# Performance work log

Hardware: AMD Instinct MI355X
Metric: run time of the kernel (lower is better)

Reference implementation:

```python
import jax, jax.numpy as jnp
import numpy as np

NUM_BINS = 256


def setup_inputs() -> dict:
    key = jax.random.key(0)
    x = jax.random.uniform(key, (16, 3, 1024, 1024), dtype=jnp.float32)
    return {"x": x}


def reference(x) -> jnp.ndarray:
    B, C, H, W = x.shape
    # Quantize to NUM_BINS levels (values in [0,1] so truncation == torch .long())
    x_flat = jnp.clip(x, 0.0, 1.0).reshape(B, C, H * W)
    x_q = jnp.clip((x_flat * (NUM_BINS - 1)).astype(jnp.int32), 0, NUM_BINS - 1)
    # Per-(B,C) histogram via a single flat scatter-add: offset each (b,c)
    # slice into its own NUM_BINS-wide segment of one 1-D buffer.
    offsets = (jnp.arange(B * C, dtype=jnp.int32) * NUM_BINS).reshape(B, C, 1)
    flat_idx = (x_q + offsets).reshape(-1)
    hist = jnp.zeros(B * C * NUM_BINS, dtype=jnp.float32).at[flat_idx].add(1.0)
    hist = hist.reshape(B, C, NUM_BINS)
    # CDF, normalized by total count (clamped at 1 to avoid div-by-zero)
    cdf = jnp.cumsum(hist, axis=2)
    cdf = cdf / jnp.maximum(cdf[:, :, -1:], 1.0)
    # Remap each pixel through its channel's CDF
    y_flat = jnp.take_along_axis(cdf, x_q, axis=2)
    return y_flat.reshape(B, C, H, W).astype(x.dtype)
```

## Files before the change

kernel.cpp:

```cpp
#include <hip/hip_runtime.h>

#define NB 256
#define NCH 48
#define HW (1024*1024)
#define BLOCKS_PER_CH 64
#define THREADS 256

__device__ __forceinline__ int quant255(float v) {
    v = fminf(fmaxf(v, 0.0f), 1.0f);
    int q = (int)(v * 255.0f);
    q = q < 0 ? 0 : q;
    q = q > 255 ? 255 : q;
    return q;
}

__global__ __launch_bounds__(THREADS) void hist_kernel(
    const float* __restrict__ x, unsigned int* __restrict__ ghist) {
    __shared__ unsigned int lh[NB];
    const int t = threadIdx.x;
    lh[t] = 0u;
    __syncthreads();

    const int ch  = blockIdx.x / BLOCKS_PER_CH;
    const int blk = blockIdx.x % BLOCKS_PER_CH;

    const float4* xp = (const float4*)(x + (size_t)ch * HW);
    const int n4_per_block = (HW / 4) / BLOCKS_PER_CH;
    const int base = blk * n4_per_block;

    for (int i = base + t; i < base + n4_per_block; i += THREADS) {
        float4 v = xp[i];
        atomicAdd(&lh[quant255(v.x)], 1u);
        atomicAdd(&lh[quant255(v.y)], 1u);
        atomicAdd(&lh[quant255(v.z)], 1u);
        atomicAdd(&lh[quant255(v.w)], 1u);
    }
    __syncthreads();
    if (lh[t] != 0u)
        atomicAdd(&ghist[ch * NB + t], lh[t]);
}

__global__ __launch_bounds__(THREADS) void cdf_kernel(
    const unsigned int* __restrict__ ghist, float* __restrict__ cdf) {
    __shared__ float s[NB];
    const int c = blockIdx.x, t = threadIdx.x;
    s[t] = (float)ghist[c * NB + t];
    __syncthreads();
    for (int off = 1; off < NB; off <<= 1) {
        float add = (t >= off) ? s[t - off] : 0.0f;
        __syncthreads();
        s[t] += add;
        __syncthreads();
    }
    float total = s[NB - 1];
    cdf[c * NB + t] = s[t] / fmaxf(total, 1.0f);
}

__global__ __launch_bounds__(THREADS) void remap_kernel(
    const float* __restrict__ x, const float* __restrict__ cdf,
    float* __restrict__ y) {
    __shared__ float lc[NB];
    const int t = threadIdx.x;
    const int ch  = blockIdx.x / BLOCKS_PER_CH;
    const int blk = blockIdx.x % BLOCKS_PER_CH;
    lc[t] = cdf[ch * NB + t];
    __syncthreads();

    const float4* xp = (const float4*)(x + (size_t)ch * HW);
    float4*       yp = (float4*)      (y + (size_t)ch * HW);
    const int n4_per_block = (HW / 4) / BLOCKS_PER_CH;
    const int base = blk * n4_per_block;

    for (int i = base + t; i < base + n4_per_block; i += THREADS) {
        float4 v = xp[i];
        float4 o;
        o.x = lc[quant255(v.x)];
        o.y = lc[quant255(v.y)];
        o.z = lc[quant255(v.z)];
        o.w = lc[quant255(v.w)];
        yp[i] = o;
    }
}

extern "C" void kernel_launch(void* const* d_in, const int* in_sizes, int n_in,
                              void* d_out, int out_size, void* d_ws, size_t ws_size,
                              hipStream_t stream) {
    const float* x = (const float*)d_in[0];
    float* y = (float*)d_out;

    unsigned int* ghist = (unsigned int*)d_ws;
    float* cdf = (float*)((char*)d_ws + NCH * NB * sizeof(unsigned int));

    hipMemsetAsync(ghist, 0, NCH * NB * sizeof(unsigned int), stream);

    hist_kernel <<<NCH * BLOCKS_PER_CH, THREADS, 0, stream>>>(x, ghist);
    cdf_kernel  <<<NCH,                 THREADS, 0, stream>>>(ghist, cdf);
    remap_kernel<<<NCH * BLOCKS_PER_CH, THREADS, 0, stream>>>(x, cdf, y);
}
```

Measured before the change: 378.2 us.

## Cache quantized bytes for remap and use per-wave shared histograms

The histogram pass now writes the 8-bit quantized values to workspace. The remap pass reads these bytes instead of re-reading and re-quantizing the float input, which cuts its read traffic by four times. Shared-memory histograms are also split per wavefront to reduce atomic contention. The cost is an extra byte write in the first pass and a dependency on a workspace large enough to hold one byte per element.

```diff
diff --git a/kernel.cpp b/kernel.cpp
--- a/kernel.cpp
+++ b/kernel.cpp
@@ -5,6 +5,7 @@
 #define HW (1024*1024)
 #define BLOCKS_PER_CH 64
 #define THREADS 256
+#define NWAVE (THREADS / 64)
 
 __device__ __forceinline__ int quant255(float v) {
     v = fminf(fmaxf(v, 0.0f), 1.0f);
@@ -14,30 +15,40 @@
     return q;
 }
 
-__global__ __launch_bounds__(THREADS) void hist_kernel(
-    const float* __restrict__ x, unsigned int* __restrict__ ghist) {
-    __shared__ unsigned int lh[NB];
+__global__ __launch_bounds__(THREADS) void hist_quant_kernel(
+    const float* __restrict__ x, unsigned int* __restrict__ ghist,
+    unsigned char* __restrict__ q) {
+    __shared__ unsigned int lh[NWAVE][NB];
     const int t = threadIdx.x;
-    lh[t] = 0u;
+    const int w = t >> 6;
+    for (int i = t; i < NWAVE * NB; i += THREADS)
+        ((unsigned int*)lh)[i] = 0u;
     __syncthreads();
 
     const int ch  = blockIdx.x / BLOCKS_PER_CH;
     const int blk = blockIdx.x % BLOCKS_PER_CH;
 
     const float4* xp = (const float4*)(x + (size_t)ch * HW);
-    const int n4_per_block = (HW / 4) / BLOCKS_PER_CH;
-    const int base = blk * n4_per_block;
+    uchar4*       qp = (uchar4*)      (q + (size_t)ch * HW);
+    const int n4 = (HW / 4) / BLOCKS_PER_CH;
+    const int base = blk * n4;
 
-    for (int i = base + t; i < base + n4_per_block; i += THREADS) {
+    for (int i = base + t; i < base + n4; i += THREADS) {
         float4 v = xp[i];
-        atomicAdd(&lh[quant255(v.x)], 1u);
-        atomicAdd(&lh[quant255(v.y)], 1u);
-        atomicAdd(&lh[quant255(v.z)], 1u);
-        atomicAdd(&lh[quant255(v.w)], 1u);
+        int q0 = quant255(v.x), q1 = quant255(v.y);
+        int q2 = quant255(v.z), q3 = quant255(v.w);
+        atomicAdd(&lh[w][q0], 1u);
+        atomicAdd(&lh[w][q1], 1u);
+        atomicAdd(&lh[w][q2], 1u);
+        atomicAdd(&lh[w][q3], 1u);
+        qp[i] = make_uchar4((unsigned char)q0, (unsigned char)q1,
+                            (unsigned char)q2, (unsigned char)q3);
     }
     __syncthreads();
-    if (lh[t] != 0u)
-        atomicAdd(&ghist[ch * NB + t], lh[t]);
+    unsigned int s = 0;
+    for (int r = 0; r < NWAVE; ++r) s += lh[r][t];
+    if (s != 0u)
+        atomicAdd(&ghist[ch * NB + t], s);
 }
 
 __global__ __launch_bounds__(THREADS) void cdf_kernel(
@@ -57,7 +68,7 @@
 }
 
 __global__ __launch_bounds__(THREADS) void remap_kernel(
-    const float* __restrict__ x, const float* __restrict__ cdf,
+    const unsigned char* __restrict__ q, const float* __restrict__ cdf,
     float* __restrict__ y) {
     __shared__ float lc[NB];
     const int t = threadIdx.x;
@@ -66,18 +77,14 @@
     lc[t] = cdf[ch * NB + t];
     __syncthreads();
 
-    const float4* xp = (const float4*)(x + (size_t)ch * HW);
+    const uchar4* qp = (const uchar4*)(q + (size_t)ch * HW);
     float4*       yp = (float4*)      (y + (size_t)ch * HW);
-    const int n4_per_block = (HW / 4) / BLOCKS_PER_CH;
-    const int base = blk * n4_per_block;
+    const int n4 = (HW / 4) / BLOCKS_PER_CH;
+    const int base = blk * n4;
 
-    for (int i = base + t; i < base + n4_per_block; i += THREADS) {
-        float4 v = xp[i];
-        float4 o;
-        o.x = lc[quant255(v.x)];
-        o.y = lc[quant255(v.y)];
-        o.z = lc[quant255(v.z)];
-        o.w = lc[quant255(v.w)];
+    for (int i = base + t; i < base + n4; i += THREADS) {
+        uchar4 v = qp[i];
+        float4 o = make_float4(lc[v.x], lc[v.y], lc[v.z], lc[v.w]);
         yp[i] = o;
     }
 }
@@ -88,12 +95,13 @@
     const float* x = (const float*)d_in[0];
     float* y = (float*)d_out;
 
-    unsigned int* ghist = (unsigned int*)d_ws;
-    float* cdf = (float*)((char*)d_ws + NCH * NB * sizeof(unsigned int));
+    unsigned int*  ghist = (unsigned int*)d_ws;
+    float*         cdf   = (float*)((char*)d_ws + NCH * NB * sizeof(unsigned int));
+    unsigned char* q     = (unsigned char*)((char*)d_ws + 256 * 1024);
 
     hipMemsetAsync(ghist, 0, NCH * NB * sizeof(unsigned int), stream);
 
-    hist_kernel <<<NCH * BLOCKS_PER_CH, THREADS, 0, stream>>>(x, ghist);
-    cdf_kernel  <<<NCH,                 THREADS, 0, stream>>>(ghist, cdf);
-    remap_kernel<<<NCH * BLOCKS_PER_CH, THREADS, 0, stream>>>(x, cdf, y);
+    hist_quant_kernel<<<NCH * BLOCKS_PER_CH, THREADS, 0, stream>>>(x, ghist, q);
+    cdf_kernel       <<<NCH,                 THREADS, 0, stream>>>(ghist, cdf);
+    remap_kernel     <<<NCH * BLOCKS_PER_CH, THREADS, 0, stream>>>(q, cdf, y);
 }
```

Result: faster. 368.6 us (-2.5%).
